# Kernel optimization log

Measured on AMD Instinct MI355X. Metric: run time of the kernel, lower is better.

The kernel has to match this reference:

```python
import jax, jax.numpy as jnp
import numpy as np

N = 100000   # nodes
E = 1600000  # edges
G = 64       # graphs in batch
H, C = 8, 16 # heads, per-head channels
HID = H * C  # 128
EMB, BBOX, TOK, REL = 256, 32, 151, 51
IN0 = EMB + BBOX  # 288
NEG_SLOPE = 0.2
BN_EPS = 1e-5


def setup_inputs() -> dict:
    key = jax.random.key(0)
    ks = jax.random.split(key, 32)
    f = lambda i, shape: jax.random.normal(ks[i], shape, dtype=jnp.float32) * 0.05
    inp = {}
    inp["tok_id"] = jax.random.randint(ks[0], (N,), 0, TOK)
    inp["bbox"] = jax.random.normal(ks[1], (N, 4), dtype=jnp.float32)
    inp["edge_index"] = jax.random.randint(ks[2], (2, E), 0, N)
    inp["edge_attr"] = jax.random.randint(ks[3], (E,), 0, REL)
    inp["batch"] = jnp.sort(jax.random.randint(ks[4], (N,), 0, G))
    inp["tok_emb"] = f(5, (TOK, EMB))
    inp["bbox_W"] = f(6, (4, BBOX)); inp["bbox_b"] = f(7, (BBOX,))
    inp["rel_emb"] = f(8, (REL, C))
    # layer 0 (in_dim 288 -> 128)
    inp["Wl0"] = f(9, (IN0, HID));  inp["bl0"] = f(10, (HID,))
    inp["Wr0"] = f(11, (IN0, HID)); inp["br0"] = f(12, (HID,))
    inp["We0"] = f(13, (C, HID));   inp["att0"] = f(14, (H, C))
    inp["bias0"] = f(15, (HID,))
    inp["gamma0"] = jnp.ones((HID,), jnp.float32); inp["beta0"] = jnp.zeros((HID,), jnp.float32)
    # layers 1..2 stacked (128 -> 128)
    inp["WlS"] = f(16, (2, HID, HID)); inp["blS"] = f(17, (2, HID))
    inp["WrS"] = f(18, (2, HID, HID)); inp["brS"] = f(19, (2, HID))
    inp["WeS"] = f(20, (2, C, HID));   inp["attS"] = f(21, (2, H, C))
    inp["biasS"] = f(22, (2, HID))
    inp["gammaS"] = jnp.ones((2, HID), jnp.float32); inp["betaS"] = jnp.zeros((2, HID), jnp.float32)
    return inp


def gatv2_layer(x, src, dst, e_emb, Wl, bl, Wr, br, We, att, bias):
    """GATv2Conv: gather -> leaky_relu attention -> segment softmax -> scatter."""
    xl = (x @ Wl + bl).reshape(-1, H, C)   # source transform [N,H,C]
    xr = (x @ Wr + br).reshape(-1, H, C)   # target transform [N,H,C]
    ee = (e_emb @ We).reshape(-1, H, C)    # edge transform  [E,H,C]
    m = jax.nn.leaky_relu(xl[src] + xr[dst] + ee, NEG_SLOPE)  # [E,H,C]
    logits = jnp.einsum('ehc,hc->eh', m, att)                 # [E,H]
    amax = jax.ops.segment_max(logits, dst, num_segments=N)   # [N,H]
    p = jnp.exp(logits - amax[dst])
    denom = jax.ops.segment_sum(p, dst, num_segments=N)       # [N,H]
    alpha = p / jnp.maximum(denom[dst], 1e-16)                # [E,H]
    out = jax.ops.segment_sum(alpha[..., None] * xl[src], dst, num_segments=N)  # [N,H,C]
    return out.reshape(-1, HID) + bias


def batch_norm(x, gamma, beta):
    mu = jnp.mean(x, axis=0)
    var = jnp.var(x, axis=0)
    return gamma * (x - mu) * jax.lax.rsqrt(var + BN_EPS) + beta


def reference(tok_id, bbox, edge_index, edge_attr, batch,
              tok_emb, bbox_W, bbox_b, rel_emb,
              Wl0, bl0, Wr0, br0, We0, att0, bias0, gamma0, beta0,
              WlS, blS, WrS, brS, WeS, attS, biasS, gammaS, betaS):
    src, dst = edge_index[0], edge_index[1]
    x = jnp.concatenate([tok_emb[tok_id], bbox @ bbox_W + bbox_b], axis=-1)  # [N,288]
    e_emb = rel_emb[edge_attr]  # [E,16]
    h = batch_norm(jax.nn.relu(
        gatv2_layer(x, src, dst, e_emb, Wl0, bl0, Wr0, br0, We0, att0, bias0)),
        gamma0, beta0)
    for i in range(2):
        h = h + batch_norm(jax.nn.relu(
            gatv2_layer(h, src, dst, e_emb, WlS[i], blS[i], WrS[i], brS[i], WeS[i], attS[i], biasS[i])),
            gammaS[i], betaS[i])
    # global mean pool over graphs
    sums = jax.ops.segment_sum(h, batch, num_segments=G)
    counts = jax.ops.segment_sum(jnp.ones((h.shape[0],), h.dtype), batch, num_segments=G)
    return sums / jnp.maximum(counts, 1.0)[:, None]  # [G,128]
```

## Files before the change

kernel.cpp:

```cpp
#include <hip/hip_runtime.h>

#define N_NODES 100000
#define N_PAD   100096
#define N_EDGES 1600000
#define NGRAPH  64
#define NHEAD   8
#define NCH     16
#define HID     128
#define IN0     288
#define NREL    51
#define EMB     256
#define NBBOX   32
#define NTOK    151
#define NEG_SLOPE 0.2f
#define EPS_BN  1e-5f
#define AGG_BLOCKS 2048
#define POOL_BLOCKS 1024
#define SENT 0x03F00000u
#define SENT_MIN ((uint)(NREL) << 20)
#define L2E 1.4426950408889634f

typedef unsigned int uint;
typedef unsigned short ushort;

typedef __bf16 bf16_t;
typedef bf16_t bfx8 __attribute__((ext_vector_type(8)));
typedef float  fx4  __attribute__((ext_vector_type(4)));
typedef float  v2f  __attribute__((ext_vector_type(2)));

__device__ __forceinline__ ushort f2bf(float f) {
  uint u = __float_as_uint(f);
  u += 0x7fffu + ((u >> 16) & 1u);
  return (ushort)(u >> 16);
}
__device__ __forceinline__ float bf2f(uint u) { return __uint_as_float(u << 16); }
__device__ __forceinline__ v2f up2(uint u) {
  v2f r;
  r.x = __uint_as_float(u << 16);
  r.y = __uint_as_float(u & 0xffff0000u);
  return r;
}
__device__ __forceinline__ void unpack8(uint4 u, float* f) {
  f[0] = __uint_as_float(u.x << 16); f[1] = __uint_as_float(u.x & 0xffff0000u);
  f[2] = __uint_as_float(u.y << 16); f[3] = __uint_as_float(u.y & 0xffff0000u);
  f[4] = __uint_as_float(u.z << 16); f[5] = __uint_as_float(u.z & 0xffff0000u);
  f[6] = __uint_as_float(u.w << 16); f[7] = __uint_as_float(u.w & 0xffff0000u);
}

__device__ __forceinline__ float w0cat(const float* Wl0, const float* Wr0, int c, int j) {
  return (j < 128) ? Wl0[c * 128 + j] : Wr0[c * 128 + (j - 128)];
}

#define S0 (2 * 256 * HID)
#define S1 (3 * NREL * HID)
#define S2 (3 * 256)
#define S3 (NTOK * 256)
#define S4 (4 * 256)
#define S5 (256)
#define PREP_TOT (S0 + S1 + S2 + S3 + S4 + S5)
__global__ void se_prep(const float* __restrict__ Wl0, const float* __restrict__ Wr0,
                        const float* __restrict__ WlS, const float* __restrict__ WrS,
                        const float* __restrict__ rel_emb, const float* __restrict__ We0,
                        const float* __restrict__ WeS,
                        const float* __restrict__ bl0, const float* __restrict__ br0,
                        const float* __restrict__ blS, const float* __restrict__ brS,
                        const float* __restrict__ tok_emb, const float* __restrict__ bbox_W,
                        const float* __restrict__ bbox_b,
                        ushort* __restrict__ WST, float* __restrict__ eetab,
                        float* __restrict__ biascat,
                        float* __restrict__ T, float* __restrict__ F, float* __restrict__ cvec) {
  int i = blockIdx.x * 256 + threadIdx.x;
  if (i < S0) {
    int li = i >> 15;
    int rem = i & 32767;
    int j = rem >> 7, k = rem & 127;
    float v = (j < 128) ? WlS[(li * 128 + k) * 128 + j] : WrS[(li * 128 + k) * 128 + (j - 128)];
    WST[(li * 256 + j) * 128 + k] = f2bf(v);
    return;
  }
  i -= S0;
  if (i < S1) {
    int li = i / (NREL * HID);
    int rem = i - li * (NREL * HID);
    int r = rem >> 7, j = rem & 127;
    const float* We = (li == 0) ? We0 : (WeS + (li - 1) * NCH * HID);
    float s = 0.f;
#pragma unroll
    for (int c = 0; c < NCH; c++) s += rel_emb[r * NCH + c] * We[c * HID + j];
    eetab[li * (NREL * HID) + rem] = s;
    return;
  }
  i -= S1;
  if (i < S2) {
    int li = i >> 8, j = i & 255;
    const float* bl = (li == 0) ? bl0 : (blS + (li - 1) * HID);
    const float* br = (li == 0) ? br0 : (brS + (li - 1) * HID);
    biascat[i] = (j < 128) ? bl[j] : br[j - 128];
    return;
  }
  i -= S2;
  if (i < S3) {
    int t = i >> 8, j = i & 255;
    float s = 0.f;
    for (int c = 0; c < EMB; c++) s += tok_emb[t * EMB + c] * w0cat(Wl0, Wr0, c, j);
    T[i] = s;
    return;
  }
  i -= S3;
  if (i < S4) {
    int r = i >> 8, j = i & 255;
    float s = 0.f;
#pragma unroll
    for (int b = 0; b < NBBOX; b++) s += bbox_W[r * NBBOX + b] * w0cat(Wl0, Wr0, EMB + b, j);
    F[i] = s;
    return;
  }
  i -= S4;
  if (i < S5) {
    int j = i;
    float s = (j < 128) ? bl0[j] : br0[j - 128];
#pragma unroll
    for (int b = 0; b < NBBOX; b++) s += bbox_b[b] * w0cat(Wl0, Wr0, EMB + b, j);
    cvec[j] = s;
  }
}

__global__ void se_xform0(const int* __restrict__ tok_id, const float* __restrict__ bbox,
                          const float* __restrict__ T, const float* __restrict__ F,
                          const float* __restrict__ cvec, ushort* __restrict__ xlxr) {
  int idx = blockIdx.x * 256 + threadIdx.x;
  if (idx >= N_NODES * 32) return;
  const int n = idx >> 5, k = idx & 31;
  const int j0 = k * 8;
  const int t = tok_id[n];
  const float4 bb = *(const float4*)(bbox + (size_t)n * 4);
  float o[8];
#pragma unroll
  for (int h = 0; h < 2; h++) {
    const float4 tv = *(const float4*)(T + t * 256 + j0 + 4 * h);
    const float4 cv = *(const float4*)(cvec + j0 + 4 * h);
    const float4 f0 = *(const float4*)(F + 0 * 256 + j0 + 4 * h);
    const float4 f1 = *(const float4*)(F + 1 * 256 + j0 + 4 * h);
    const float4 f2 = *(const float4*)(F + 2 * 256 + j0 + 4 * h);
    const float4 f3 = *(const float4*)(F + 3 * 256 + j0 + 4 * h);
    o[4 * h + 0] = tv.x + cv.x + bb.x * f0.x + bb.y * f1.x + bb.z * f2.x + bb.w * f3.x;
    o[4 * h + 1] = tv.y + cv.y + bb.x * f0.y + bb.y * f1.y + bb.z * f2.y + bb.w * f3.y;
    o[4 * h + 2] = tv.z + cv.z + bb.x * f0.z + bb.y * f1.z + bb.z * f2.z + bb.w * f3.z;
    o[4 * h + 3] = tv.w + cv.w + bb.x * f0.w + bb.y * f1.w + bb.z * f2.w + bb.w * f3.w;
  }
  uint4 p;
  p.x = ((uint)f2bf(o[1]) << 16) | f2bf(o[0]);
  p.y = ((uint)f2bf(o[3]) << 16) | f2bf(o[2]);
  p.z = ((uint)f2bf(o[5]) << 16) | f2bf(o[4]);
  p.w = ((uint)f2bf(o[7]) << 16) | f2bf(o[6]);
  ((uint4*)xlxr)[idx] = p;
}

__global__ void se_hist(const int* __restrict__ ei, int* __restrict__ deg) {
  int e = blockIdx.x * 256 + threadIdx.x;
  if (e < N_EDGES) atomicAdd(&deg[ei[N_EDGES + e]], 1);
}
__global__ __launch_bounds__(1024) void se_scanA(const int* __restrict__ deg,
                                                 int* __restrict__ offs, int* __restrict__ bsum) {
  __shared__ int s[1024];
  const int tid = threadIdx.x;
  const int i = blockIdx.x * 1024 + tid;
  int v = (i < N_NODES) ? ((deg[i] + 3) & ~3) : 0;
  s[tid] = v;
  __syncthreads();
  for (int d = 1; d < 1024; d <<= 1) {
    int t = (tid >= d) ? s[tid - d] : 0;
    __syncthreads();
    s[tid] += t;
    __syncthreads();
  }
  if (i < N_NODES) offs[i] = s[tid] - v;
  if (tid == 1023) bsum[blockIdx.x] = s[1023];
}
__global__ __launch_bounds__(128) void se_scanB(int* __restrict__ bsum, int nb) {
  __shared__ int s[128];
  const int t = threadIdx.x;
  int v = (t < nb) ? bsum[t] : 0;
  s[t] = v;
  __syncthreads();
  for (int d = 1; d < 128; d <<= 1) {
    int u = (t >= d) ? s[t - d] : 0;
    __syncthreads();
    s[t] += u;
    __syncthreads();
  }
  if (t < nb) bsum[t] = s[t] - v;
}
__global__ __launch_bounds__(1024) void se_scanC_pad(int* __restrict__ offs,
                                                     const int* __restrict__ bsum,
                                                     const int* __restrict__ deg,
                                                     uint* __restrict__ csrp,
                                                     int2* __restrict__ rowinfo) {
  int i = blockIdx.x * 1024 + threadIdx.x;
  if (i >= N_NODES) return;
  const int o = offs[i] + bsum[blockIdx.x];
  offs[i] = o;
  const int d = deg[i];
  rowinfo[i] = make_int2(o, (d + 3) >> 2);
  const int s = o + d;
  const int c = ((d + 3) & ~3) - d;
  for (int j = 0; j < c; j++) csrp[s + j] = SENT;
  if (i == N_NODES - 1) {
    const int e = o + ((d + 3) & ~3);
    for (int j = 0; j < 64; j++) csrp[e + j] = SENT;
  }
}
__global__ void se_scatter(const int* __restrict__ ei, const int* __restrict__ eattr,
                           const int* __restrict__ offs, int* __restrict__ cur,
                           uint* __restrict__ csrp) {
  int e = blockIdx.x * 256 + threadIdx.x;
  if (e < N_EDGES) {
    int d = ei[N_EDGES + e];
    int p = offs[d] + atomicAdd(&cur[d], 1);
    csrp[p] = (uint)ei[e] | ((uint)eattr[e] << 20);
  }
}

template <int K>
__global__ __launch_bounds__(256) void se_gemm(const ushort* __restrict__ A,
                                               const ushort* __restrict__ BT,
                                               const float* __restrict__ bias,
                                               ushort* __restrict__ C) {
  __shared__ __align__(16) ushort As[128 * 32];
  __shared__ __align__(16) ushort Bs[128 * 32];
  const int tid = threadIdx.x;
  const int w = tid >> 6, l = tid & 63;
  const int wr = w >> 1, wc = w & 1;
  const int m0 = blockIdx.x * 128, n0 = blockIdx.y * 128;
  fx4 acc[4][4];
#pragma unroll
  for (int i = 0; i < 4; i++)
#pragma unroll
    for (int j = 0; j < 4; j++) acc[i][j] = fx4{0.f, 0.f, 0.f, 0.f};

  for (int k0 = 0; k0 < K; k0 += 32) {
#pragma unroll
    for (int ch = 0; ch < 2; ch++) {
      const int t = tid + ch * 256;
      const int r = t >> 2, c = (t & 3) << 3;
      const ushort* ga = A + (size_t)(m0 + r) * K + (k0 + c);
      ushort* la = As + (size_t)(ch * 256 + w * 64) * 8;
      __builtin_amdgcn_global_load_lds((const __attribute__((address_space(1))) void*)ga,
                                       (__attribute__((address_space(3))) void*)la, 16, 0, 0);
      const ushort* gb = BT + (size_t)(n0 + r) * K + (k0 + c);
      ushort* lb = Bs + (size_t)(ch * 256 + w * 64) * 8;
      __builtin_amdgcn_global_load_lds((const __attribute__((address_space(1))) void*)gb,
                                       (__attribute__((address_space(3))) void*)lb, 16, 0, 0);
    }
    __syncthreads();
    bfx8 af[4], bfr[4];
#pragma unroll
    for (int i = 0; i < 4; i++) {
      af[i]  = *(const bfx8*)(As + ((wr * 64 + i * 16 + (l & 15)) * 32 + ((l >> 4) * 8)));
      bfr[i] = *(const bfx8*)(Bs + ((wc * 64 + i * 16 + (l & 15)) * 32 + ((l >> 4) * 8)));
    }
#pragma unroll
    for (int i = 0; i < 4; i++)
#pragma unroll
      for (int j = 0; j < 4; j++)
        acc[i][j] = __builtin_amdgcn_mfma_f32_16x16x32_bf16(af[i], bfr[j], acc[i][j], 0, 0, 0);
    __syncthreads();
  }
#pragma unroll
  for (int i = 0; i < 4; i++) {
    const int rbase = m0 + wr * 64 + i * 16 + ((l >> 4) << 2);
#pragma unroll
    for (int j = 0; j < 4; j++) {
      const int col = n0 + wc * 64 + j * 16 + (l & 15);
      const float bz = bias[col];
#pragma unroll
      for (int r2 = 0; r2 < 4; r2++) {
        const int row = rbase + r2;
        if (row < N_NODES) C[(size_t)row * 256 + col] = f2bf(acc[i][j][r2] + bz);
      }
    }
  }
}

__global__ __launch_bounds__(256) void se_agg(const uint4* __restrict__ xlxr4,
                                              const uint* __restrict__ csrp,
                                              const int2* __restrict__ rowinfo,
                                              const float* __restrict__ eetab,
                                              const float* __restrict__ att,
                                              const float* __restrict__ bias,
                                              float* __restrict__ y, float* __restrict__ partial) {
  __shared__ ushort ee[64 * HID];
  __shared__ float bstat[256];
  const int tid = threadIdx.x, w = tid >> 6, l = tid & 63;
  const int g = l >> 4, k = l & 15;
  for (int i = tid; i < 64 * HID; i += 256) {
    const int r = i >> 7;
    ee[i] = (r < NREL) ? f2bf(eetab[i]) : (ushort)0;
  }
  bstat[tid] = 0.f;
  __syncthreads();
  v2f av[4];
  {
    const float* ap = att + (k >> 1) * NCH + (k & 1) * 8;
#pragma unroll
    for (int q = 0; q < 4; q++) av[q] = v2f{ap[2 * q] * L2E, ap[2 * q + 1] * L2E};
  }
  v2f sv[4], qv[4];
#pragma unroll
  for (int q = 0; q < 4; q++) { sv[q] = v2f{0.f, 0.f}; qv[q] = v2f{0.f, 0.f}; }
  const v2f zero = v2f{0.f, 0.f};

  const int stride = gridDim.x * 4;
  int n = blockIdx.x * 4 + w;
  int2 ri = make_int2(0, 0);
  uint eA = SENT;
  uint4 xlv = uint4{0u, 0u, 0u, 0u};
  if (n < N_NODES) {
    ri = rowinfo[n];
    eA = csrp[ri.x + g];
    xlv = xlxr4[(eA & 0xFFFFFu) * 32u + (uint)k];
  }
  while (n < N_NODES) {
    const int n2 = n + stride;
    int2 ri2 = make_int2(0, 0);
    if (n2 < N_NODES) ri2 = rowinfo[n2];
    const uint4 xru = xlxr4[(uint)n * 32u + 16u + (uint)k];
    const uint* rowp = csrp + ri.x + g;
    const int nit = ri.y;
    uint eB = SENT;
    if (nit > 1) eB = rowp[4];
    v2f xrv[4];
    xrv[0] = up2(xru.x); xrv[1] = up2(xru.y); xrv[2] = up2(xru.z); xrv[3] = up2(xru.w);
    float den = 0.f;
    v2f acc[4];
#pragma unroll
    for (int q = 0; q < 4; q++) acc[q] = zero;

    for (int i = 0; i < nit; ++i) {
      const uint ec = eA;
      const uint4 xc = xlv;
      eA = eB;
      if (i + 1 < nit) xlv = xlxr4[(eA & 0xFFFFFu) * 32u + (uint)k];
      if (i + 2 < nit) eB = rowp[4 * (i + 2)];
      const uint4 eeu = *(const uint4*)(ee + (ec >> 20) * HID + k * 8);
      v2f sd = zero;
      v2f xls[4];
      {
        const uint xcu[4] = {xc.x, xc.y, xc.z, xc.w};
        const uint eu[4] = {eeu.x, eeu.y, eeu.z, eeu.w};
#pragma unroll
        for (int q = 0; q < 4; q++) {
          const v2f xl = up2(xcu[q]);
          const v2f m = xl + xrv[q] + up2(eu[q]);
          const v2f lk = __builtin_elementwise_max(m, NEG_SLOPE * m);
          sd += lk * av[q];
          xls[q] = xl;
        }
      }
      float s = sd.x + sd.y;
      s += __shfl_xor(s, 1);
      s = (ec >= SENT_MIN) ? -1e30f : s;
      const float p = exp2f(s);
      den += p;
      const v2f pp = v2f{p, p};
#pragma unroll
      for (int q = 0; q < 4; q++) acc[q] += pp * xls[q];
    }
    uint eA2 = SENT;
    if (n2 < N_NODES) eA2 = csrp[ri2.x + g];
    den += __shfl_xor(den, 16);
    den += __shfl_xor(den, 32);
#pragma unroll
    for (int q = 0; q < 4; q++) {
      acc[q].x += __shfl_xor(acc[q].x, 16); acc[q].x += __shfl_xor(acc[q].x, 32);
      acc[q].y += __shfl_xor(acc[q].y, 16); acc[q].y += __shfl_xor(acc[q].y, 32);
    }
    uint4 xlv2 = uint4{0u, 0u, 0u, 0u};
    if (n2 < N_NODES) xlv2 = xlxr4[(eA2 & 0xFFFFFu) * 32u + (uint)k];
    if (g == 0) {
      const float r = 1.f / fmaxf(den, 1e-16f);
      const v2f rr = v2f{r, r};
      const float4 b0 = ((const float4*)bias)[k * 2];
      const float4 b1 = ((const float4*)bias)[k * 2 + 1];
      const v2f bv[4] = {v2f{b0.x, b0.y}, v2f{b0.z, b0.w}, v2f{b1.x, b1.y}, v2f{b1.z, b1.w}};
      v2f ov[4];
#pragma unroll
      for (int q = 0; q < 4; q++) {
        ov[q] = __builtin_elementwise_max(acc[q] * rr + bv[q], zero);
        sv[q] += ov[q];
        qv[q] += ov[q] * ov[q];
      }
      float4* yp = (float4*)y + (size_t)n * 32 + (size_t)k * 2;
      yp[0] = make_float4(ov[0].x, ov[0].y, ov[1].x, ov[1].y);
      yp[1] = make_float4(ov[2].x, ov[2].y, ov[3].x, ov[3].y);
    }
    n = n2; ri = ri2; eA = eA2; xlv = xlv2;
  }
  if (l < 16) {
#pragma unroll
    for (int q = 0; q < 4; q++) {
      unsafeAtomicAdd(&bstat[k * 8 + 2 * q], sv[q].x);
      unsafeAtomicAdd(&bstat[k * 8 + 2 * q + 1], sv[q].y);
      unsafeAtomicAdd(&bstat[128 + k * 8 + 2 * q], qv[q].x);
      unsafeAtomicAdd(&bstat[128 + k * 8 + 2 * q + 1], qv[q].y);
    }
  }
  __syncthreads();
  partial[(size_t)tid * AGG_BLOCKS + blockIdx.x] = bstat[tid];
}

__global__ __launch_bounds__(256) void se_stats(const float* __restrict__ partial, float* __restrict__ musig) {
  __shared__ float red[256];
  const int ch = blockIdx.x, tid = threadIdx.x;
  float s = 0.f;
  for (int i = tid; i < AGG_BLOCKS; i += 256) s += partial[ch * AGG_BLOCKS + i];
  red[tid] = s; __syncthreads();
  for (int o = 128; o > 0; o >>= 1) { if (tid < o) red[tid] += red[tid + o]; __syncthreads(); }
  const float sum = red[0]; __syncthreads();
  float q = 0.f;
  for (int i = tid; i < AGG_BLOCKS; i += 256) q += partial[(128 + ch) * AGG_BLOCKS + i];
  red[tid] = q; __syncthreads();
  for (int o = 128; o > 0; o >>= 1) { if (tid < o) red[tid] += red[tid + o]; __syncthreads(); }
  if (tid == 0) {
    const float mean = sum / (float)N_NODES;
    const float var = red[0] / (float)N_NODES - mean * mean;
    musig[ch] = mean;
    musig[128 + ch] = rsqrtf(var + EPS_BN);
  }
}

__global__ void se_bn(const float* __restrict__ y, const float* __restrict__ musig,
                      const float* __restrict__ gamma, const float* __restrict__ beta,
                      ushort* __restrict__ h_bf, int residual) {
  int idx = blockIdx.x * 256 + threadIdx.x;
  if (idx >= N_NODES * 16) return;
  const int k = idx & 15;
  const float4 y0 = ((const float4*)y)[(size_t)idx * 2];
  const float4 y1 = ((const float4*)y)[(size_t)idx * 2 + 1];
  const float4 mu0 = ((const float4*)musig)[k * 2],         mu1 = ((const float4*)musig)[k * 2 + 1];
  const float4 rs0 = ((const float4*)(musig + 128))[k * 2], rs1 = ((const float4*)(musig + 128))[k * 2 + 1];
  const float4 g0  = ((const float4*)gamma)[k * 2],         g1  = ((const float4*)gamma)[k * 2 + 1];
  const float4 b0  = ((const float4*)beta)[k * 2],          b1  = ((const float4*)beta)[k * 2 + 1];
  float v[8];
  v[0] = g0.x * (y0.x - mu0.x) * rs0.x + b0.x;
  v[1] = g0.y * (y0.y - mu0.y) * rs0.y + b0.y;
  v[2] = g0.z * (y0.z - mu0.z) * rs0.z + b0.z;
  v[3] = g0.w * (y0.w - mu0.w) * rs0.w + b0.w;
  v[4] = g1.x * (y1.x - mu1.x) * rs1.x + b1.x;
  v[5] = g1.y * (y1.y - mu1.y) * rs1.y + b1.y;
  v[6] = g1.z * (y1.z - mu1.z) * rs1.z + b1.z;
  v[7] = g1.w * (y1.w - mu1.w) * rs1.w + b1.w;
  if (residual) {
    const uint4 ho = ((const uint4*)h_bf)[idx];
    float fr[8];
    unpack8(ho, fr);
#pragma unroll
    for (int j = 0; j < 8; j++) v[j] += fr[j];
  }
  uint4 p4;
  p4.x = ((uint)f2bf(v[1]) << 16) | f2bf(v[0]);
  p4.y = ((uint)f2bf(v[3]) << 16) | f2bf(v[2]);
  p4.z = ((uint)f2bf(v[5]) << 16) | f2bf(v[4]);
  p4.w = ((uint)f2bf(v[7]) << 16) | f2bf(v[6]);
  ((uint4*)h_bf)[idx] = p4;
}

__global__ __launch_bounds__(256) void se_pool(const ushort* __restrict__ h_bf,
                                               const int* __restrict__ batch,
                                               float* __restrict__ pool) {
  const int tid = threadIdx.x, w = tid >> 6, l = tid & 63;
  const int wid = blockIdx.x * 4 + w;
  const int nw = gridDim.x * 4;
  const int chunk = (N_NODES + nw - 1) / nw;
  const int start = wid * chunk;
  const int end = min(N_NODES, start + chunk);
  float a0 = 0.f, a1 = 0.f;
  int cg = -1, cnt = 0;
  for (int n = start; n < end; ++n) {
    const int gg = batch[n];
    if (gg != cg) {
      if (cg >= 0) {
        unsafeAtomicAdd(&pool[cg * HID + 2 * l], a0);
        unsafeAtomicAdd(&pool[cg * HID + 2 * l + 1], a1);
        if (l == 0) unsafeAtomicAdd(&pool[NGRAPH * HID + cg], (float)cnt);
      }
      a0 = 0.f; a1 = 0.f; cnt = 0; cg = gg;
    }
    const uint u = ((const uint*)h_bf)[(size_t)n * 64 + l];
    a0 += bf2f(u & 0xffffu);
    a1 += __uint_as_float(u & 0xffff0000u);
    cnt++;
  }
  if (cg >= 0) {
    unsafeAtomicAdd(&pool[cg * HID + 2 * l], a0);
    unsafeAtomicAdd(&pool[cg * HID + 2 * l + 1], a1);
    if (l == 0) unsafeAtomicAdd(&pool[NGRAPH * HID + cg], (float)cnt);
  }
}
__global__ void se_poolfin(const float* __restrict__ pool, float* __restrict__ out) {
  int idx = blockIdx.x * 256 + threadIdx.x;
  if (idx < NGRAPH * HID) {
    int g = idx >> 7;
    out[idx] = pool[idx] / fmaxf(pool[NGRAPH * HID + g], 1.f);
  }
}

extern "C" void kernel_launch(void* const* d_in, const int* in_sizes, int n_in,
                              void* d_out, int out_size, void* d_ws, size_t ws_size,
                              hipStream_t stream) {
  (void)in_sizes; (void)n_in; (void)out_size; (void)ws_size;
  const int*   tok_id  = (const int*)d_in[0];
  const float* bbox    = (const float*)d_in[1];
  const int*   ei      = (const int*)d_in[2];
  const int*   eattr   = (const int*)d_in[3];
  const int*   batch   = (const int*)d_in[4];
  const float* tok_emb = (const float*)d_in[5];
  const float* bbox_W  = (const float*)d_in[6];
  const float* bbox_b  = (const float*)d_in[7];
  const float* rel_emb = (const float*)d_in[8];
  const float* Wl0  = (const float*)d_in[9];
  const float* bl0  = (const float*)d_in[10];
  const float* Wr0  = (const float*)d_in[11];
  const float* br0  = (const float*)d_in[12];
  const float* We0  = (const float*)d_in[13];
  const float* att0 = (const float*)d_in[14];
  const float* bias0  = (const float*)d_in[15];
  const float* gamma0 = (const float*)d_in[16];
  const float* beta0  = (const float*)d_in[17];
  const float* WlS  = (const float*)d_in[18];
  const float* blS  = (const float*)d_in[19];
  const float* WrS  = (const float*)d_in[20];
  const float* brS  = (const float*)d_in[21];
  const float* WeS  = (const float*)d_in[22];
  const float* attS = (const float*)d_in[23];
  const float* biasS  = (const float*)d_in[24];
  const float* gammaS = (const float*)d_in[25];
  const float* betaS  = (const float*)d_in[26];
  float* out = (float*)d_out;

  char* ws = (char*)d_ws;
  size_t off = 0;
  auto alloc = [&](size_t bytes) -> char* {
    char* p = ws + off;
    off = (off + bytes + 255) & ~(size_t)255;
    return p;
  };
  ushort* xlxr = (ushort*)alloc((size_t)N_PAD * 256 * 2);
  float*  y    = (float*)alloc((size_t)N_NODES * HID * 4);
  ushort* h_bf = (ushort*)alloc((size_t)N_PAD * HID * 2);
  ushort* WST  = (ushort*)alloc((size_t)2 * 256 * HID * 2);
  float*  eetab   = (float*)alloc((size_t)3 * NREL * HID * 4);
  float*  biascat = (float*)alloc((size_t)3 * 256 * 4);
  float*  T    = (float*)alloc((size_t)NTOK * 256 * 4);
  float*  F    = (float*)alloc((size_t)4 * 256 * 4);
  float*  cvec = (float*)alloc((size_t)256 * 4);
  char*  z0   = ws + off;
  int*   deg  = (int*)alloc((size_t)N_NODES * 4);
  int*   cur  = (int*)alloc((size_t)N_NODES * 4);
  float* pool = (float*)alloc((size_t)(NGRAPH * HID + NGRAPH) * 4);
  size_t zlen = (size_t)((ws + off) - z0);
  int* offs = (int*)alloc((size_t)(N_NODES + 1) * 4);
  int* bsum = (int*)alloc(128 * 4);
  int2* rowinfo = (int2*)alloc((size_t)N_NODES * 8);
  uint* csrp = (uint*)alloc((size_t)(N_EDGES + 3 * N_NODES + 256) * 4);
  float* partial = (float*)alloc((size_t)256 * AGG_BLOCKS * 4);
  float* musig   = (float*)alloc(256 * 4);

  hipMemsetAsync(z0, 0, zlen, stream);

  se_prep<<<(PREP_TOT + 255) / 256, 256, 0, stream>>>(
      Wl0, Wr0, WlS, WrS, rel_emb, We0, WeS, bl0, br0, blS, brS,
      tok_emb, bbox_W, bbox_b, WST, eetab, biascat, T, F, cvec);
  se_hist<<<(N_EDGES + 255) / 256, 256, 0, stream>>>(ei, deg);
  se_scanA<<<98, 1024, 0, stream>>>(deg, offs, bsum);
  se_scanB<<<1, 128, 0, stream>>>(bsum, 98);
  se_scanC_pad<<<98, 1024, 0, stream>>>(offs, bsum, deg, csrp, rowinfo);
  se_scatter<<<(N_EDGES + 255) / 256, 256, 0, stream>>>(ei, eattr, offs, cur, csrp);

  se_xform0<<<(N_NODES * 32 + 255) / 256, 256, 0, stream>>>(tok_id, bbox, T, F, cvec, xlxr);
  se_agg<<<AGG_BLOCKS, 256, 0, stream>>>((const uint4*)xlxr, csrp, rowinfo,
                                         eetab, att0, bias0, y, partial);
  se_stats<<<128, 256, 0, stream>>>(partial, musig);
  se_bn<<<(N_NODES * 16 + 255) / 256, 256, 0, stream>>>(y, musig, gamma0, beta0, h_bf, 0);

  for (int li = 0; li < 2; ++li) {
    se_gemm<HID><<<dim3(N_PAD / 128, 2), 256, 0, stream>>>(h_bf, WST + (size_t)li * 256 * HID,
                                                           biascat + (li + 1) * 256, xlxr);
    se_agg<<<AGG_BLOCKS, 256, 0, stream>>>((const uint4*)xlxr, csrp, rowinfo,
                                           eetab + (size_t)(li + 1) * NREL * HID,
                                           attS + (size_t)li * NHEAD * NCH,
                                           biasS + (size_t)li * HID, y, partial);
    se_stats<<<128, 256, 0, stream>>>(partial, musig);
    se_bn<<<(N_NODES * 16 + 255) / 256, 256, 0, stream>>>(y, musig, gammaS + (size_t)li * HID,
                                                          betaS + (size_t)li * HID, h_bf, 1);
  }

  se_pool<<<POOL_BLOCKS, 256, 0, stream>>>(h_bf, batch, pool);
  se_poolfin<<<32, 256, 0, stream>>>(pool, out);
}
```

Baseline: 810.7 us.

## Use nontemporal loads/stores, atomic BN stats, and in-place scatter offsets

Several unrelated tweaks land together. se_scatter now does its atomicAdd directly on offs, which drops the separate cur array. se_agg reads CSR, rowinfo and the xr rows with nontemporal loads and writes y with nontemporal stores, and se_bn reads y nontemporally, all to limit cache pollution. The per-block BN partials and the 128-block reduction are replaced by float atomics into 8 striped accumulators plus a tiny single-block stats kernel, with the accumulators re-zeroed by a memset before each later layer. The atomics make the statistics summation order nondeterministic. After scatter, offs holds row end positions rather than row starts, but rowinfo was already written, so nothing breaks.

```diff
diff --git a/kernel.cpp b/kernel.cpp
--- a/kernel.cpp
+++ b/kernel.cpp
@@ -27,6 +27,7 @@
 typedef bf16_t bfx8 __attribute__((ext_vector_type(8)));
 typedef float  fx4  __attribute__((ext_vector_type(4)));
 typedef float  v2f  __attribute__((ext_vector_type(2)));
+typedef uint   ux4  __attribute__((ext_vector_type(4)));
 
 __device__ __forceinline__ ushort f2bf(float f) {
   uint u = __float_as_uint(f);
@@ -211,12 +212,11 @@
   }
 }
 __global__ void se_scatter(const int* __restrict__ ei, const int* __restrict__ eattr,
-                           const int* __restrict__ offs, int* __restrict__ cur,
-                           uint* __restrict__ csrp) {
+                           int* __restrict__ offs, uint* __restrict__ csrp) {
   int e = blockIdx.x * 256 + threadIdx.x;
   if (e < N_EDGES) {
     int d = ei[N_EDGES + e];
-    int p = offs[d] + atomicAdd(&cur[d], 1);
+    int p = atomicAdd(&offs[d], 1);
     csrp[p] = (uint)ei[e] | ((uint)eattr[e] << 20);
   }
 }
@@ -284,11 +284,11 @@
 
 __global__ __launch_bounds__(256) void se_agg(const uint4* __restrict__ xlxr4,
                                               const uint* __restrict__ csrp,
-                                              const int2* __restrict__ rowinfo,
+                                              const long long* __restrict__ rowinfo,
                                               const float* __restrict__ eetab,
                                               const float* __restrict__ att,
                                               const float* __restrict__ bias,
-                                              float* __restrict__ y, float* __restrict__ partial) {
+                                              float* __restrict__ y, float* __restrict__ macc) {
   __shared__ ushort ee[64 * HID];
   __shared__ float bstat[256];
   const int tid = threadIdx.x, w = tid >> 6, l = tid & 63;
@@ -312,23 +312,27 @@
 
   const int stride = gridDim.x * 4;
   int n = blockIdx.x * 4 + w;
-  int2 ri = make_int2(0, 0);
+  int riO = 0, riN = 0;
   uint eA = SENT;
   uint4 xlv = uint4{0u, 0u, 0u, 0u};
   if (n < N_NODES) {
-    ri = rowinfo[n];
-    eA = csrp[ri.x + g];
+    const long long rl = __builtin_nontemporal_load(rowinfo + n);
+    riO = (int)rl; riN = (int)(rl >> 32);
+    eA = __builtin_nontemporal_load(csrp + riO + g);
     xlv = xlxr4[(eA & 0xFFFFFu) * 32u + (uint)k];
   }
   while (n < N_NODES) {
     const int n2 = n + stride;
-    int2 ri2 = make_int2(0, 0);
-    if (n2 < N_NODES) ri2 = rowinfo[n2];
-    const uint4 xru = xlxr4[(uint)n * 32u + 16u + (uint)k];
-    const uint* rowp = csrp + ri.x + g;
-    const int nit = ri.y;
+    int riO2 = 0, riN2 = 0;
+    if (n2 < N_NODES) {
+      const long long rl2 = __builtin_nontemporal_load(rowinfo + n2);
+      riO2 = (int)rl2; riN2 = (int)(rl2 >> 32);
+    }
+    const ux4 xru = __builtin_nontemporal_load((const ux4*)xlxr4 + ((uint)n * 32u + 16u + (uint)k));
+    const uint* rowp = csrp + riO + g;
+    const int nit = riN;
     uint eB = SENT;
-    if (nit > 1) eB = rowp[4];
+    if (nit > 1) eB = __builtin_nontemporal_load(rowp + 4);
     v2f xrv[4];
     xrv[0] = up2(xru.x); xrv[1] = up2(xru.y); xrv[2] = up2(xru.z); xrv[3] = up2(xru.w);
     float den = 0.f;
@@ -341,7 +345,7 @@
       const uint4 xc = xlv;
       eA = eB;
       if (i + 1 < nit) xlv = xlxr4[(eA & 0xFFFFFu) * 32u + (uint)k];
-      if (i + 2 < nit) eB = rowp[4 * (i + 2)];
+      if (i + 2 < nit) eB = __builtin_nontemporal_load(rowp + 4 * (i + 2));
       const uint4 eeu = *(const uint4*)(ee + (ec >> 20) * HID + k * 8);
       v2f sd = zero;
       v2f xls[4];
@@ -367,7 +371,7 @@
       for (int q = 0; q < 4; q++) acc[q] += pp * xls[q];
     }
     uint eA2 = SENT;
-    if (n2 < N_NODES) eA2 = csrp[ri2.x + g];
+    if (n2 < N_NODES) eA2 = __builtin_nontemporal_load(csrp + riO2 + g);
     den += __shfl_xor(den, 16);
     den += __shfl_xor(den, 32);
 #pragma unroll
@@ -390,11 +394,11 @@
         sv[q] += ov[q];
         qv[q] += ov[q] * ov[q];
       }
-      float4* yp = (float4*)y + (size_t)n * 32 + (size_t)k * 2;
-      yp[0] = make_float4(ov[0].x, ov[0].y, ov[1].x, ov[1].y);
-      yp[1] = make_float4(ov[2].x, ov[2].y, ov[3].x, ov[3].y);
-    }
-    n = n2; ri = ri2; eA = eA2; xlv = xlv2;
+      fx4* yp = (fx4*)y + (size_t)n * 32 + (size_t)k * 2;
+      __builtin_nontemporal_store(fx4{ov[0].x, ov[0].y, ov[1].x, ov[1].y}, yp);
+      __builtin_nontemporal_store(fx4{ov[2].x, ov[2].y, ov[3].x, ov[3].y}, yp + 1);
+    }
+    n = n2; riO = riO2; riN = riN2; eA = eA2; xlv = xlv2;
   }
   if (l < 16) {
 #pragma unroll
@@ -406,27 +410,21 @@
     }
   }
   __syncthreads();
-  partial[(size_t)tid * AGG_BLOCKS + blockIdx.x] = bstat[tid];
-}
-
-__global__ __launch_bounds__(256) void se_stats(const float* __restrict__ partial, float* __restrict__ musig) {
-  __shared__ float red[256];
-  const int ch = blockIdx.x, tid = threadIdx.x;
-  float s = 0.f;
-  for (int i = tid; i < AGG_BLOCKS; i += 256) s += partial[ch * AGG_BLOCKS + i];
-  red[tid] = s; __syncthreads();
-  for (int o = 128; o > 0; o >>= 1) { if (tid < o) red[tid] += red[tid + o]; __syncthreads(); }
-  const float sum = red[0]; __syncthreads();
-  float q = 0.f;
-  for (int i = tid; i < AGG_BLOCKS; i += 256) q += partial[(128 + ch) * AGG_BLOCKS + i];
-  red[tid] = q; __syncthreads();
-  for (int o = 128; o > 0; o >>= 1) { if (tid < o) red[tid] += red[tid + o]; __syncthreads(); }
-  if (tid == 0) {
-    const float mean = sum / (float)N_NODES;
-    const float var = red[0] / (float)N_NODES - mean * mean;
-    musig[ch] = mean;
-    musig[128 + ch] = rsqrtf(var + EPS_BN);
-  }
+  unsafeAtomicAdd(&macc[(size_t)(blockIdx.x & 7) * 256 + tid], bstat[tid]);
+}
+
+__global__ __launch_bounds__(128) void se_stats(const float* __restrict__ macc, float* __restrict__ musig) {
+  const int ch = threadIdx.x;
+  float sum = 0.f, sq = 0.f;
+#pragma unroll
+  for (int b = 0; b < 8; b++) {
+    sum += macc[b * 256 + ch];
+    sq  += macc[b * 256 + 128 + ch];
+  }
+  const float mean = sum / (float)N_NODES;
+  const float var = sq / (float)N_NODES - mean * mean;
+  musig[ch] = mean;
+  musig[128 + ch] = rsqrtf(var + EPS_BN);
 }
 
 __global__ void se_bn(const float* __restrict__ y, const float* __restrict__ musig,
@@ -435,8 +433,8 @@
   int idx = blockIdx.x * 256 + threadIdx.x;
   if (idx >= N_NODES * 16) return;
   const int k = idx & 15;
-  const float4 y0 = ((const float4*)y)[(size_t)idx * 2];
-  const float4 y1 = ((const float4*)y)[(size_t)idx * 2 + 1];
+  const fx4 y0 = __builtin_nontemporal_load((const fx4*)y + (size_t)idx * 2);
+  const fx4 y1 = __builtin_nontemporal_load((const fx4*)y + (size_t)idx * 2 + 1);
   const float4 mu0 = ((const float4*)musig)[k * 2],         mu1 = ((const float4*)musig)[k * 2 + 1];
   const float4 rs0 = ((const float4*)(musig + 128))[k * 2], rs1 = ((const float4*)(musig + 128))[k * 2 + 1];
   const float4 g0  = ((const float4*)gamma)[k * 2],         g1  = ((const float4*)gamma)[k * 2 + 1];
@@ -556,14 +554,13 @@
   float*  cvec = (float*)alloc((size_t)256 * 4);
   char*  z0   = ws + off;
   int*   deg  = (int*)alloc((size_t)N_NODES * 4);
-  int*   cur  = (int*)alloc((size_t)N_NODES * 4);
+  float* macc = (float*)alloc((size_t)8 * 256 * 4);
   float* pool = (float*)alloc((size_t)(NGRAPH * HID + NGRAPH) * 4);
   size_t zlen = (size_t)((ws + off) - z0);
   int* offs = (int*)alloc((size_t)(N_NODES + 1) * 4);
   int* bsum = (int*)alloc(128 * 4);
   int2* rowinfo = (int2*)alloc((size_t)N_NODES * 8);
   uint* csrp = (uint*)alloc((size_t)(N_EDGES + 3 * N_NODES + 256) * 4);
-  float* partial = (float*)alloc((size_t)256 * AGG_BLOCKS * 4);
   float* musig   = (float*)alloc(256 * 4);
 
   hipMemsetAsync(z0, 0, zlen, stream);
@@ -575,22 +572,23 @@
   se_scanA<<<98, 1024, 0, stream>>>(deg, offs, bsum);
   se_scanB<<<1, 128, 0, stream>>>(bsum, 98);
   se_scanC_pad<<<98, 1024, 0, stream>>>(offs, bsum, deg, csrp, rowinfo);
-  se_scatter<<<(N_EDGES + 255) / 256, 256, 0, stream>>>(ei, eattr, offs, cur, csrp);
+  se_scatter<<<(N_EDGES + 255) / 256, 256, 0, stream>>>(ei, eattr, offs, csrp);
 
   se_xform0<<<(N_NODES * 32 + 255) / 256, 256, 0, stream>>>(tok_id, bbox, T, F, cvec, xlxr);
-  se_agg<<<AGG_BLOCKS, 256, 0, stream>>>((const uint4*)xlxr, csrp, rowinfo,
-                                         eetab, att0, bias0, y, partial);
-  se_stats<<<128, 256, 0, stream>>>(partial, musig);
+  se_agg<<<AGG_BLOCKS, 256, 0, stream>>>((const uint4*)xlxr, csrp, (const long long*)rowinfo,
+                                         eetab, att0, bias0, y, macc);
+  se_stats<<<1, 128, 0, stream>>>(macc, musig);
   se_bn<<<(N_NODES * 16 + 255) / 256, 256, 0, stream>>>(y, musig, gamma0, beta0, h_bf, 0);
 
   for (int li = 0; li < 2; ++li) {
+    hipMemsetAsync(macc, 0, (size_t)8 * 256 * 4, stream);
     se_gemm<HID><<<dim3(N_PAD / 128, 2), 256, 0, stream>>>(h_bf, WST + (size_t)li * 256 * HID,
                                                            biascat + (li + 1) * 256, xlxr);
-    se_agg<<<AGG_BLOCKS, 256, 0, stream>>>((const uint4*)xlxr, csrp, rowinfo,
+    se_agg<<<AGG_BLOCKS, 256, 0, stream>>>((const uint4*)xlxr, csrp, (const long long*)rowinfo,
                                            eetab + (size_t)(li + 1) * NREL * HID,
                                            attS + (size_t)li * NHEAD * NCH,
-                                           biasS + (size_t)li * HID, y, partial);
-    se_stats<<<128, 256, 0, stream>>>(partial, musig);
+                                           biasS + (size_t)li * HID, y, macc);
+    se_stats<<<1, 128, 0, stream>>>(macc, musig);
     se_bn<<<(N_NODES * 16 + 255) / 256, 256, 0, stream>>>(y, musig, gammaS + (size_t)li * HID,
                                                           betaS + (size_t)li * HID, h_bf, 1);
   }
```

New measurement: 873.9 us. +7.8%, slower.
